# Kernel optimization log

Measured on AMD Instinct MI355X. Metric: run time of the kernel, lower is better.

Reference implementation:

```python
import jax, jax.numpy as jnp
import numpy as np

NUM_NODES = 20000
NUM_EDGES = 65536
WIDTH = 64
EDGE_FEAT = 6
HIDDEN = 128


def setup_inputs() -> dict:
    key = jax.random.key(0)
    ks = jax.random.split(key, 6)
    x = jax.random.normal(ks[0], (NUM_NODES, WIDTH), dtype=jnp.float32)
    edge_attr = jax.random.normal(ks[1], (NUM_EDGES, EDGE_FEAT), dtype=jnp.float32)
    # weight-generating MLP params (the `nn` callable), fan-in scaled
    W1 = jax.random.normal(ks[2], (EDGE_FEAT, HIDDEN), dtype=jnp.float32) / np.sqrt(EDGE_FEAT)
    b1 = jnp.zeros((HIDDEN,), dtype=jnp.float32)
    W2 = jax.random.normal(ks[3], (HIDDEN, WIDTH * WIDTH), dtype=jnp.float32) / np.sqrt(HIDDEN)
    b2 = jnp.zeros((WIDTH * WIDTH,), dtype=jnp.float32)
    senders = jax.random.randint(ks[4], (NUM_EDGES,), 0, NUM_NODES)
    receivers = jax.random.randint(ks[5], (NUM_EDGES,), 0, NUM_NODES)
    return {"x": x, "edge_attr": edge_attr, "W1": W1, "b1": b1,
            "W2": W2, "b2": b2, "senders": senders, "receivers": receivers}


def reference(x, edge_attr, W1, b1, W2, b2, senders, receivers):
    n_segs, width = x.shape
    # nn(edge_attr): (E, width*width) edge-conditioned weights
    h = jax.nn.relu(edge_attr @ W1 + b1)
    weight = (h @ W2 + b2).reshape(-1, width, width)  # (E, w, w)
    # gather sender features, per-edge (1,w) @ (w,w) matmul -> (E, w)
    msgs = jnp.einsum('ew,ewv->ev', x[senders], weight)
    # scatter-sum messages into receiver nodes (aggr == 'sum')
    return jax.ops.segment_sum(msgs, receivers, num_segments=n_segs)
```

## Files before the change

### kernel.cpp

```cpp
#include <hip/hip_runtime.h>
#include <stdint.h>

typedef _Float16 f16;
typedef f16 f16x8 __attribute__((ext_vector_type(8)));
typedef float f32x4 __attribute__((ext_vector_type(4)));

#define NUM_NODES 20000
#define NUM_EDGES 65536
#define WIDTH 64
#define EDGE_FEAT 6
#define HIDDEN 128
#define BM 256
#define NCHUNK 129
#define XPAD 72

#define XH_HALFS (NUM_NODES * WIDTH)
#define XCONV_BLKS 625

__global__ __launch_bounds__(256) void prep_kernel(
    const float* __restrict__ x, const float* __restrict__ W2,
    const float* __restrict__ b2, f16* __restrict__ ws_h)
{
  __shared__ float row[4096];
  f16* x_h = ws_h;
  f16* W2g = ws_h + XH_HALFS;
  const int blk = blockIdx.x, tid = threadIdx.x;

  if (blk < NCHUNK) {
    const int ki = blk;
    const float* srcrow;
    if (ki < HIDDEN) {
      const float4* src = (const float4*)(W2 + (size_t)ki * 4096);
      #pragma unroll
      for (int i = 0; i < 4; ++i) {
        float4 v = src[tid + 256 * i];
        *(float4*)&row[(tid + 256 * i) * 4] = v;
      }
      __syncthreads();
      srcrow = row;
    } else {
      srcrow = b2;
    }
    const int obase = tid * 16;
    f16x8 outv0, outv1;
    #pragma unroll
    for (int u = 0; u < 8; ++u) {
      int o = obase + u;
      int n = o >> 6, pg = (o >> 3) & 7, j = o & 7;
      int k = (pg ^ (n & 7)) * 8 + j;
      outv0[u] = (f16)srcrow[k * 64 + n];
    }
    #pragma unroll
    for (int u = 0; u < 8; ++u) {
      int o = obase + 8 + u;
      int n = o >> 6, pg = (o >> 3) & 7, j = o & 7;
      int k = (pg ^ (n & 7)) * 8 + j;
      outv1[u] = (f16)srcrow[k * 64 + n];
    }
    *(f16x8*)&W2g[(size_t)ki * 4096 + obase] = outv0;
    *(f16x8*)&W2g[(size_t)ki * 4096 + obase + 8] = outv1;
  } else {
    int idx = (blk - NCHUNK) * 2048 + tid * 8;
    if (idx + 8 <= XH_HALFS) {
      float4 a = *(const float4*)(x + idx);
      float4 b = *(const float4*)(x + idx + 4);
      f16x8 hv;
      hv[0] = (f16)a.x; hv[1] = (f16)a.y; hv[2] = (f16)a.z; hv[3] = (f16)a.w;
      hv[4] = (f16)b.x; hv[5] = (f16)b.y; hv[6] = (f16)b.z; hv[7] = (f16)b.w;
      *(f16x8*)&x_h[idx] = hv;
    }
  }
}

__global__ __launch_bounds__(256, 2) void nnconv_kernel(
    const float* __restrict__ ea, const float* __restrict__ W1,
    const float* __restrict__ b1, const int* __restrict__ senders,
    const int* __restrict__ receivers, const f16* __restrict__ ws_h,
    float* __restrict__ out)
{
  const f16* x_h = ws_h;
  const f16* W2g = ws_h + XH_HALFS;
  __shared__ __align__(16) f16 xt[BM][XPAD];
  __shared__ __align__(16) f16 Bb[2][4096];

  const int tid = threadIdx.x;
  const int lane = tid & 63, wid = tid >> 6;
  const int quad = lane >> 4, l15 = lane & 15;
  const int chunk = blockIdx.x & 255;
  const int khalf = blockIdx.x >> 8;
  const int k0 = khalf ? 65 : 0;
  const int kcount = khalf ? 64 : 65;
  const int e0 = chunk * BM;
  const int rowbase = wid * 64;

  {
    int s = senders[e0 + tid];
    const uint4* src = (const uint4*)(x_h + (size_t)s * WIDTH);
    uint4* dst = (uint4*)&xt[tid][0];
    #pragma unroll
    for (int i = 0; i < 8; ++i) dst[i] = src[i];
  }

  float ear[4][6];
  #pragma unroll
  for (int t = 0; t < 4; ++t) {
    const float* p = ea + (size_t)(e0 + rowbase + t * 16 + l15) * EDGE_FEAT;
    #pragma unroll
    for (int f = 0; f < 6; ++f) ear[t][f] = p[f];
  }

  int boff[2][4];
  #pragma unroll
  for (int kc = 0; kc < 2; ++kc)
    #pragma unroll
    for (int nt = 0; nt < 4; ++nt) {
      int n = nt * 16 + l15;
      int g = kc * 4 + quad;
      boff[kc][nt] = n * 64 + (g ^ (n & 7)) * 8;
    }

  uint4 pre0 = *(const uint4*)(W2g + (size_t)k0 * 4096 + tid * 8);
  uint4 pre1 = *(const uint4*)(W2g + (size_t)k0 * 4096 + 2048 + tid * 8);

  __syncthreads();

  f16x8 xf[4][2];
  #pragma unroll
  for (int t = 0; t < 4; ++t)
    #pragma unroll
    for (int kc = 0; kc < 2; ++kc)
      xf[t][kc] = *(const f16x8*)&xt[rowbase + t * 16 + l15][kc * 32 + quad * 8];

  f32x4 acc[4][4];
  #pragma unroll
  for (int t = 0; t < 4; ++t)
    #pragma unroll
    for (int nt = 0; nt < 4; ++nt)
      acc[t][nt] = (f32x4){0.f, 0.f, 0.f, 0.f};

  for (int kk = 0; kk < kcount; ++kk) {
    const int ki = k0 + kk;
    f16* buf = &Bb[kk & 1][0];
    *(uint4*)&buf[tid * 8] = pre0;
    *(uint4*)&buf[2048 + tid * 8] = pre1;
    if (kk + 1 < kcount) {
      pre0 = *(const uint4*)(W2g + (size_t)(ki + 1) * 4096 + tid * 8);
      pre1 = *(const uint4*)(W2g + (size_t)(ki + 1) * 4096 + 2048 + tid * 8);
    }

    f16 hv[4];
    if (ki < HIDDEN) {
      float b1c = b1[ki];
      float w1c[6];
      #pragma unroll
      for (int f = 0; f < 6; ++f) w1c[f] = W1[f * HIDDEN + ki];
      #pragma unroll
      for (int t = 0; t < 4; ++t) {
        float s = b1c;
        #pragma unroll
        for (int f = 0; f < 6; ++f) s = fmaf(ear[t][f], w1c[f], s);
        hv[t] = (f16)fmaxf(s, 0.f);
      }
    } else {
      #pragma unroll
      for (int t = 0; t < 4; ++t) hv[t] = (f16)1.f;
    }

    __syncthreads();

    f16x8 bf[2][4];
    #pragma unroll
    for (int kc = 0; kc < 2; ++kc)
      #pragma unroll
      for (int nt = 0; nt < 4; ++nt)
        bf[kc][nt] = *(const f16x8*)&buf[boff[kc][nt]];

    #pragma unroll
    for (int t = 0; t < 4; ++t) {
      f16x8 sa0 = xf[t][0] * hv[t];
      f16x8 sa1 = xf[t][1] * hv[t];
      #pragma unroll
      for (int nt = 0; nt < 4; ++nt) {
        acc[t][nt] = __builtin_amdgcn_mfma_f32_16x16x32_f16(sa0, bf[0][nt], acc[t][nt], 0, 0, 0);
        acc[t][nt] = __builtin_amdgcn_mfma_f32_16x16x32_f16(sa1, bf[1][nt], acc[t][nt], 0, 0, 0);
      }
    }
  }

  #pragma unroll
  for (int t = 0; t < 4; ++t) {
    int ebase = e0 + rowbase + t * 16 + quad * 4;
    int rc[4];
    #pragma unroll
    for (int r = 0; r < 4; ++r) rc[r] = receivers[ebase + r];
    #pragma unroll
    for (int nt = 0; nt < 4; ++nt) {
      int v = nt * 16 + l15;
      #pragma unroll
      for (int r = 0; r < 4; ++r)
        atomicAdd(out + (size_t)rc[r] * WIDTH + v, acc[t][nt][r]);
    }
  }
}

extern "C" void kernel_launch(void* const* d_in, const int* in_sizes, int n_in,
                              void* d_out, int out_size, void* d_ws, size_t ws_size,
                              hipStream_t stream) {
  const float* x  = (const float*)d_in[0];
  const float* ea = (const float*)d_in[1];
  const float* W1 = (const float*)d_in[2];
  const float* b1 = (const float*)d_in[3];
  const float* W2 = (const float*)d_in[4];
  const float* b2 = (const float*)d_in[5];
  const int* snd  = (const int*)d_in[6];
  const int* rcv  = (const int*)d_in[7];
  float* out = (float*)d_out;
  f16* wsh = (f16*)d_ws;

  hipMemsetAsync(d_out, 0, (size_t)out_size * sizeof(float), stream);
  prep_kernel<<<NCHUNK + XCONV_BLKS, 256, 0, stream>>>(x, W2, b2, wsh);
  nnconv_kernel<<<2 * (NUM_EDGES / BM), 256, 0, stream>>>(ea, W1, b1, snd, rcv, wsh, out);
}
```

Before: 150.8 us.

## Precompute hidden activations in prep pass and stream W2 fragments directly to registers

```diff
diff --git a/kernel.cpp b/kernel.cpp
--- a/kernel.cpp
+++ b/kernel.cpp
@@ -16,17 +16,23 @@
 
 #define XH_HALFS (NUM_NODES * WIDTH)
 #define XCONV_BLKS 625
+#define W2G_HALFS (NCHUNK * 4096)
+#define HT_HALFS ((size_t)NCHUNK * NUM_EDGES)
+#define HBLKS (NUM_EDGES / 256)
 
 __global__ __launch_bounds__(256) void prep_kernel(
     const float* __restrict__ x, const float* __restrict__ W2,
-    const float* __restrict__ b2, f16* __restrict__ ws_h)
+    const float* __restrict__ b2, const float* __restrict__ ea,
+    const float* __restrict__ W1, const float* __restrict__ b1,
+    f16* __restrict__ ws_h)
 {
-  __shared__ float row[4096];
   f16* x_h = ws_h;
   f16* W2g = ws_h + XH_HALFS;
+  f16* hT  = ws_h + XH_HALFS + W2G_HALFS;
   const int blk = blockIdx.x, tid = threadIdx.x;
 
   if (blk < NCHUNK) {
+    __shared__ float row[4096];
     const int ki = blk;
     const float* srcrow;
     if (ki < HIDDEN) {
@@ -59,7 +65,7 @@
     }
     *(f16x8*)&W2g[(size_t)ki * 4096 + obase] = outv0;
     *(f16x8*)&W2g[(size_t)ki * 4096 + obase + 8] = outv1;
-  } else {
+  } else if (blk < NCHUNK + XCONV_BLKS) {
     int idx = (blk - NCHUNK) * 2048 + tid * 8;
     if (idx + 8 <= XH_HALFS) {
       float4 a = *(const float4*)(x + idx);
@@ -69,9 +75,29 @@
       hv[4] = (f16)b.x; hv[5] = (f16)b.y; hv[6] = (f16)b.z; hv[7] = (f16)b.w;
       *(f16x8*)&x_h[idx] = hv;
     }
+  } else {
+    __shared__ float w1s[EDGE_FEAT * HIDDEN];
+    __shared__ float b1s[HIDDEN];
+    for (int i = tid; i < EDGE_FEAT * HIDDEN; i += 256) w1s[i] = W1[i];
+    if (tid < HIDDEN) b1s[tid] = b1[tid];
+    __syncthreads();
+    const int e = (blk - NCHUNK - XCONV_BLKS) * 256 + tid;
+    const float* p = ea + (size_t)e * EDGE_FEAT;
+    float a[6];
+    #pragma unroll
+    for (int f = 0; f < 6; ++f) a[f] = p[f];
+    #pragma unroll 4
+    for (int k = 0; k < HIDDEN; ++k) {
+      float s = b1s[k];
+      #pragma unroll
+      for (int f = 0; f < 6; ++f) s = fmaf(a[f], w1s[f * HIDDEN + k], s);
+      hT[(size_t)k * NUM_EDGES + e] = (f16)fmaxf(s, 0.f);
+    }
+    hT[(size_t)HIDDEN * NUM_EDGES + e] = (f16)1.f;
   }
 }
 
+template<int HT>
 __global__ __launch_bounds__(256, 2) void nnconv_kernel(
     const float* __restrict__ ea, const float* __restrict__ W1,
     const float* __restrict__ b1, const int* __restrict__ senders,
@@ -80,8 +106,8 @@
 {
   const f16* x_h = ws_h;
   const f16* W2g = ws_h + XH_HALFS;
+  const f16* hT  = ws_h + XH_HALFS + W2G_HALFS;
   __shared__ __align__(16) f16 xt[BM][XPAD];
-  __shared__ __align__(16) f16 Bb[2][4096];
 
   const int tid = threadIdx.x;
   const int lane = tid & 63, wid = tid >> 6;
@@ -102,11 +128,13 @@
   }
 
   float ear[4][6];
-  #pragma unroll
-  for (int t = 0; t < 4; ++t) {
-    const float* p = ea + (size_t)(e0 + rowbase + t * 16 + l15) * EDGE_FEAT;
-    #pragma unroll
-    for (int f = 0; f < 6; ++f) ear[t][f] = p[f];
+  if (!HT) {
+    #pragma unroll
+    for (int t = 0; t < 4; ++t) {
+      const float* p = ea + (size_t)(e0 + rowbase + t * 16 + l15) * EDGE_FEAT;
+      #pragma unroll
+      for (int f = 0; f < 6; ++f) ear[t][f] = p[f];
+    }
   }
 
   int boff[2][4];
@@ -119,8 +147,23 @@
       boff[kc][nt] = n * 64 + (g ^ (n & 7)) * 8;
     }
 
-  uint4 pre0 = *(const uint4*)(W2g + (size_t)k0 * 4096 + tid * 8);
-  uint4 pre1 = *(const uint4*)(W2g + (size_t)k0 * 4096 + 2048 + tid * 8);
+  const int hrow = e0 + rowbase + l15;
+
+  f16x8 bc[2][4];
+  f16 hc[4];
+  {
+    const f16* Bp = W2g + (size_t)k0 * 4096;
+    #pragma unroll
+    for (int kc = 0; kc < 2; ++kc)
+      #pragma unroll
+      for (int nt = 0; nt < 4; ++nt)
+        bc[kc][nt] = *(const f16x8*)(Bp + boff[kc][nt]);
+    if (HT) {
+      const f16* hp = hT + (size_t)k0 * NUM_EDGES + hrow;
+      #pragma unroll
+      for (int t = 0; t < 4; ++t) hc[t] = hp[t * 16];
+    }
+  }
 
   __syncthreads();
 
@@ -140,40 +183,46 @@
 
   for (int kk = 0; kk < kcount; ++kk) {
     const int ki = k0 + kk;
-    f16* buf = &Bb[kk & 1][0];
-    *(uint4*)&buf[tid * 8] = pre0;
-    *(uint4*)&buf[2048 + tid * 8] = pre1;
-    if (kk + 1 < kcount) {
-      pre0 = *(const uint4*)(W2g + (size_t)(ki + 1) * 4096 + tid * 8);
-      pre1 = *(const uint4*)(W2g + (size_t)(ki + 1) * 4096 + 2048 + tid * 8);
+    const int kin = (kk + 1 < kcount) ? ki + 1 : ki;
+
+    f16x8 bn[2][4];
+    f16 hn[4];
+    {
+      const f16* Bp = W2g + (size_t)kin * 4096;
+      #pragma unroll
+      for (int kc = 0; kc < 2; ++kc)
+        #pragma unroll
+        for (int nt = 0; nt < 4; ++nt)
+          bn[kc][nt] = *(const f16x8*)(Bp + boff[kc][nt]);
+      if (HT) {
+        const f16* hp = hT + (size_t)kin * NUM_EDGES + hrow;
+        #pragma unroll
+        for (int t = 0; t < 4; ++t) hn[t] = hp[t * 16];
+      }
     }
 
     f16 hv[4];
-    if (ki < HIDDEN) {
-      float b1c = b1[ki];
-      float w1c[6];
-      #pragma unroll
-      for (int f = 0; f < 6; ++f) w1c[f] = W1[f * HIDDEN + ki];
-      #pragma unroll
-      for (int t = 0; t < 4; ++t) {
-        float s = b1c;
-        #pragma unroll
-        for (int f = 0; f < 6; ++f) s = fmaf(ear[t][f], w1c[f], s);
-        hv[t] = (f16)fmaxf(s, 0.f);
-      }
+    if (HT) {
+      #pragma unroll
+      for (int t = 0; t < 4; ++t) hv[t] = hc[t];
     } else {
-      #pragma unroll
-      for (int t = 0; t < 4; ++t) hv[t] = (f16)1.f;
-    }
-
-    __syncthreads();
-
-    f16x8 bf[2][4];
-    #pragma unroll
-    for (int kc = 0; kc < 2; ++kc)
-      #pragma unroll
-      for (int nt = 0; nt < 4; ++nt)
-        bf[kc][nt] = *(const f16x8*)&buf[boff[kc][nt]];
+      if (ki < HIDDEN) {
+        float b1c = b1[ki];
+        float w1c[6];
+        #pragma unroll
+        for (int f = 0; f < 6; ++f) w1c[f] = W1[f * HIDDEN + ki];
+        #pragma unroll
+        for (int t = 0; t < 4; ++t) {
+          float s = b1c;
+          #pragma unroll
+          for (int f = 0; f < 6; ++f) s = fmaf(ear[t][f], w1c[f], s);
+          hv[t] = (f16)fmaxf(s, 0.f);
+        }
+      } else {
+        #pragma unroll
+        for (int t = 0; t < 4; ++t) hv[t] = (f16)1.f;
+      }
+    }
 
     #pragma unroll
     for (int t = 0; t < 4; ++t) {
@@ -181,9 +230,19 @@
       f16x8 sa1 = xf[t][1] * hv[t];
       #pragma unroll
       for (int nt = 0; nt < 4; ++nt) {
-        acc[t][nt] = __builtin_amdgcn_mfma_f32_16x16x32_f16(sa0, bf[0][nt], acc[t][nt], 0, 0, 0);
-        acc[t][nt] = __builtin_amdgcn_mfma_f32_16x16x32_f16(sa1, bf[1][nt], acc[t][nt], 0, 0, 0);
-      }
+        acc[t][nt] = __builtin_amdgcn_mfma_f32_16x16x32_f16(sa0, bc[0][nt], acc[t][nt], 0, 0, 0);
+        acc[t][nt] = __builtin_amdgcn_mfma_f32_16x16x32_f16(sa1, bc[1][nt], acc[t][nt], 0, 0, 0);
+      }
+    }
+
+    #pragma unroll
+    for (int kc = 0; kc < 2; ++kc)
+      #pragma unroll
+      for (int nt = 0; nt < 4; ++nt)
+        bc[kc][nt] = bn[kc][nt];
+    if (HT) {
+      #pragma unroll
+      for (int t = 0; t < 4; ++t) hc[t] = hn[t];
     }
   }
 
@@ -217,7 +276,14 @@
   float* out = (float*)d_out;
   f16* wsh = (f16*)d_ws;
 
+  const size_t need = ((size_t)XH_HALFS + W2G_HALFS + HT_HALFS) * sizeof(f16);
+  const int use_ht = (ws_size >= need) ? 1 : 0;
+
   hipMemsetAsync(d_out, 0, (size_t)out_size * sizeof(float), stream);
-  prep_kernel<<<NCHUNK + XCONV_BLKS, 256, 0, stream>>>(x, W2, b2, wsh);
-  nnconv_kernel<<<2 * (NUM_EDGES / BM), 256, 0, stream>>>(ea, W1, b1, snd, rcv, wsh, out);
+  const int prep_grid = NCHUNK + XCONV_BLKS + (use_ht ? HBLKS : 0);
+  prep_kernel<<<prep_grid, 256, 0, stream>>>(x, W2, b2, ea, W1, b1, wsh);
+  if (use_ht)
+    nnconv_kernel<1><<<2 * (NUM_EDGES / BM), 256, 0, stream>>>(ea, W1, b1, snd, rcv, wsh, out);
+  else
+    nnconv_kernel<0><<<2 * (NUM_EDGES / BM), 256, 0, stream>>>(ea, W1, b1, snd, rcv, wsh, out);
 }
```

Measured after the change: 176.5 us. 1.17x slower.

## Restructure NNConv main loop with 8-wave blocks and async LDS staging of W2

Applied to the files above, without the earlier changes.

```diff
diff --git a/kernel.cpp b/kernel.cpp
--- a/kernel.cpp
+++ b/kernel.cpp
@@ -11,23 +11,41 @@
 #define EDGE_FEAT 6
 #define HIDDEN 128
 #define BM 256
-#define NCHUNK 129
+#define PADCH 132
 #define XPAD 72
 
 #define XH_HALFS (NUM_NODES * WIDTH)
 #define XCONV_BLKS 625
+#define W2G_HALFS (PADCH * 4096)
+#define OUT_FLOATS (NUM_NODES * WIDTH)
+#define ZBLKS 313
+
+__device__ __forceinline__ void gload_lds16(const f16* g, f16* l) {
+  __builtin_amdgcn_global_load_lds(
+      (const __attribute__((address_space(1))) unsigned int*)g,
+      (__attribute__((address_space(3))) unsigned int*)l, 16, 0, 0);
+}
 
 __global__ __launch_bounds__(256) void prep_kernel(
     const float* __restrict__ x, const float* __restrict__ W2,
-    const float* __restrict__ b2, f16* __restrict__ ws_h)
+    const float* __restrict__ b2, f16* __restrict__ ws_h,
+    float* __restrict__ out)
 {
-  __shared__ float row[4096];
   f16* x_h = ws_h;
   f16* W2g = ws_h + XH_HALFS;
   const int blk = blockIdx.x, tid = threadIdx.x;
 
-  if (blk < NCHUNK) {
+  if (blk < PADCH) {
     const int ki = blk;
+    if (ki > HIDDEN) {
+      f16x8 z;
+      #pragma unroll
+      for (int u = 0; u < 8; ++u) z[u] = (f16)0.f;
+      *(f16x8*)&W2g[(size_t)ki * 4096 + tid * 16] = z;
+      *(f16x8*)&W2g[(size_t)ki * 4096 + tid * 16 + 8] = z;
+      return;
+    }
+    __shared__ float row[4096];
     const float* srcrow;
     if (ki < HIDDEN) {
       const float4* src = (const float4*)(W2 + (size_t)ki * 4096);
@@ -59,8 +77,8 @@
     }
     *(f16x8*)&W2g[(size_t)ki * 4096 + obase] = outv0;
     *(f16x8*)&W2g[(size_t)ki * 4096 + obase + 8] = outv1;
-  } else {
-    int idx = (blk - NCHUNK) * 2048 + tid * 8;
+  } else if (blk < PADCH + XCONV_BLKS) {
+    int idx = (blk - PADCH) * 2048 + tid * 8;
     if (idx + 8 <= XH_HALFS) {
       float4 a = *(const float4*)(x + idx);
       float4 b = *(const float4*)(x + idx + 4);
@@ -69,10 +87,18 @@
       hv[4] = (f16)b.x; hv[5] = (f16)b.y; hv[6] = (f16)b.z; hv[7] = (f16)b.w;
       *(f16x8*)&x_h[idx] = hv;
     }
-  }
-}
-
-__global__ __launch_bounds__(256, 2) void nnconv_kernel(
+  } else {
+    int base = (blk - PADCH - XCONV_BLKS) * 4096 + tid * 16;
+    float4 z = {0.f, 0.f, 0.f, 0.f};
+    #pragma unroll
+    for (int i = 0; i < 4; ++i) {
+      int idx = base + i * 4;
+      if (idx + 4 <= OUT_FLOATS) *(float4*)(out + idx) = z;
+    }
+  }
+}
+
+__global__ __launch_bounds__(512, 1) void nnconv_kernel(
     const float* __restrict__ ea, const float* __restrict__ W1,
     const float* __restrict__ b1, const int* __restrict__ senders,
     const int* __restrict__ receivers, const f16* __restrict__ ws_h,
@@ -81,47 +107,53 @@
   const f16* x_h = ws_h;
   const f16* W2g = ws_h + XH_HALFS;
   __shared__ __align__(16) f16 xt[BM][XPAD];
-  __shared__ __align__(16) f16 Bb[2][4096];
+  __shared__ __align__(16) f16 Bring[2 * 16384];
 
   const int tid = threadIdx.x;
   const int lane = tid & 63, wid = tid >> 6;
   const int quad = lane >> 4, l15 = lane & 15;
-  const int chunk = blockIdx.x & 255;
-  const int khalf = blockIdx.x >> 8;
-  const int k0 = khalf ? 65 : 0;
-  const int kcount = khalf ? 64 : 65;
-  const int e0 = chunk * BM;
-  const int rowbase = wid * 64;
+  const int mquad = wid >> 1, nhalf = wid & 1;
+  const int e0 = blockIdx.x * BM;
+  const int mbase = mquad * 64;
+  f16* BrF = &Bring[0];
+
+#define STAGE(GIDX, GP)                                                       \
+  {                                                                           \
+    _Pragma("unroll") for (int i_ = 0; i_ < 4; ++i_) {                        \
+      int slice_ = wid + 8 * i_;                                              \
+      gload_lds16(W2g + (size_t)(GIDX) * 16384 + slice_ * 512 + (lane << 3),  \
+                  BrF + (GP) * 16384 + slice_ * 512);                         \
+    }                                                                         \
+  }
+  STAGE(0, 0);
 
   {
-    int s = senders[e0 + tid];
-    const uint4* src = (const uint4*)(x_h + (size_t)s * WIDTH);
-    uint4* dst = (uint4*)&xt[tid][0];
-    #pragma unroll
-    for (int i = 0; i < 8; ++i) dst[i] = src[i];
+    int r = tid >> 1, half = tid & 1;
+    int s = senders[e0 + r];
+    const uint4* src = (const uint4*)(x_h + (size_t)s * WIDTH + half * 32);
+    uint4* dst = (uint4*)&xt[r][half * 32];
+    #pragma unroll
+    for (int i = 0; i < 4; ++i) dst[i] = src[i];
   }
 
   float ear[4][6];
   #pragma unroll
   for (int t = 0; t < 4; ++t) {
-    const float* p = ea + (size_t)(e0 + rowbase + t * 16 + l15) * EDGE_FEAT;
+    const float* p = ea + (size_t)(e0 + mbase + t * 16 + l15) * EDGE_FEAT;
     #pragma unroll
     for (int f = 0; f < 6; ++f) ear[t][f] = p[f];
   }
 
-  int boff[2][4];
+  int boff[2][2];
   #pragma unroll
   for (int kc = 0; kc < 2; ++kc)
     #pragma unroll
-    for (int nt = 0; nt < 4; ++nt) {
-      int n = nt * 16 + l15;
+    for (int nt = 0; nt < 2; ++nt) {
+      int n = (nhalf * 2 + nt) * 16 + l15;
       int g = kc * 4 + quad;
       boff[kc][nt] = n * 64 + (g ^ (n & 7)) * 8;
     }
 
-  uint4 pre0 = *(const uint4*)(W2g + (size_t)k0 * 4096 + tid * 8);
-  uint4 pre1 = *(const uint4*)(W2g + (size_t)k0 * 4096 + 2048 + tid * 8);
-
   __syncthreads();
 
   f16x8 xf[4][2];
@@ -129,73 +161,105 @@
   for (int t = 0; t < 4; ++t)
     #pragma unroll
     for (int kc = 0; kc < 2; ++kc)
-      xf[t][kc] = *(const f16x8*)&xt[rowbase + t * 16 + l15][kc * 32 + quad * 8];
-
-  f32x4 acc[4][4];
+      xf[t][kc] = *(const f16x8*)&xt[mbase + t * 16 + l15][kc * 32 + quad * 8];
+
+  f32x4 acc[4][2];
   #pragma unroll
   for (int t = 0; t < 4; ++t)
     #pragma unroll
-    for (int nt = 0; nt < 4; ++nt)
+    for (int nt = 0; nt < 2; ++nt)
       acc[t][nt] = (f32x4){0.f, 0.f, 0.f, 0.f};
 
-  for (int kk = 0; kk < kcount; ++kk) {
-    const int ki = k0 + kk;
-    f16* buf = &Bb[kk & 1][0];
-    *(uint4*)&buf[tid * 8] = pre0;
-    *(uint4*)&buf[2048 + tid * 8] = pre1;
-    if (kk + 1 < kcount) {
-      pre0 = *(const uint4*)(W2g + (size_t)(ki + 1) * 4096 + tid * 8);
-      pre1 = *(const uint4*)(W2g + (size_t)(ki + 1) * 4096 + 2048 + tid * 8);
-    }
-
-    f16 hv[4];
-    if (ki < HIDDEN) {
-      float b1c = b1[ki];
-      float w1c[6];
-      #pragma unroll
-      for (int f = 0; f < 6; ++f) w1c[f] = W1[f * HIDDEN + ki];
-      #pragma unroll
-      for (int t = 0; t < 4; ++t) {
-        float s = b1c;
-        #pragma unroll
-        for (int f = 0; f < 6; ++f) s = fmaf(ear[t][f], w1c[f], s);
-        hv[t] = (f16)fmaxf(s, 0.f);
+#define RD(DST, CBASE)                                                        \
+  _Pragma("unroll") for (int kc = 0; kc < 2; ++kc)                            \
+    _Pragma("unroll") for (int nt = 0; nt < 2; ++nt)                          \
+      DST[kc][nt] = *(const f16x8*)&(CBASE)[boff[kc][nt]];
+
+#define MM(BF, HV)                                                            \
+  __builtin_amdgcn_s_setprio(1);                                              \
+  _Pragma("unroll") for (int t = 0; t < 4; ++t) {                             \
+    f16x8 sa0_ = xf[t][0] * HV[t];                                            \
+    f16x8 sa1_ = xf[t][1] * HV[t];                                            \
+    _Pragma("unroll") for (int nt = 0; nt < 2; ++nt) {                        \
+      acc[t][nt] = __builtin_amdgcn_mfma_f32_16x16x32_f16(                    \
+          sa0_, BF[0][nt], acc[t][nt], 0, 0, 0);                              \
+      acc[t][nt] = __builtin_amdgcn_mfma_f32_16x16x32_f16(                    \
+          sa1_, BF[1][nt], acc[t][nt], 0, 0, 0);                              \
+    }                                                                         \
+  }                                                                           \
+  __builtin_amdgcn_s_setprio(0);
+
+#define HCOMP(KI, HV)                                                         \
+  {                                                                           \
+    float b1c_ = b1[(KI)];                                                    \
+    float w1c_[6];                                                            \
+    _Pragma("unroll") for (int f = 0; f < 6; ++f)                             \
+      w1c_[f] = W1[f * HIDDEN + (KI)];                                        \
+    _Pragma("unroll") for (int t = 0; t < 4; ++t) {                           \
+      float s_ = b1c_;                                                        \
+      _Pragma("unroll") for (int f = 0; f < 6; ++f)                           \
+        s_ = fmaf(ear[t][f], w1c_[f], s_);                                    \
+      HV[t] = (f16)fmaxf(s_, 0.f);                                            \
+    }                                                                         \
+  }
+
+  #pragma unroll 1
+  for (int g = 0; g < 32; ++g) {
+    asm volatile("s_waitcnt vmcnt(0) lgkmcnt(0)\n\ts_barrier" ::: "memory");
+    __builtin_amdgcn_sched_barrier(0);
+    STAGE(g + 1, (g + 1) & 1);
+    __builtin_amdgcn_sched_barrier(0);
+
+    f16* gb = BrF + (g & 1) * 16384;
+    const int kb = g * 4;
+    f16 h0[4], h1[4], h2[4], h3[4];
+    HCOMP(kb + 0, h0);
+    HCOMP(kb + 1, h1);
+    HCOMP(kb + 2, h2);
+    HCOMP(kb + 3, h3);
+
+    f16x8 bfP[2][2], bfQ[2][2];
+    RD(bfP, gb);
+    RD(bfQ, gb + 4096);
+    MM(bfP, h0);
+    RD(bfP, gb + 8192);
+    MM(bfQ, h1);
+    RD(bfQ, gb + 12288);
+    MM(bfP, h2);
+    MM(bfQ, h3);
+  }
+
+  asm volatile("s_waitcnt vmcnt(0) lgkmcnt(0)\n\ts_barrier" ::: "memory");
+  __builtin_amdgcn_sched_barrier(0);
+  {
+    f16x8 bfP[2][2];
+    RD(bfP, BrF);
+    __builtin_amdgcn_s_setprio(1);
+    #pragma unroll
+    for (int t = 0; t < 4; ++t)
+      #pragma unroll
+      for (int nt = 0; nt < 2; ++nt) {
+        acc[t][nt] = __builtin_amdgcn_mfma_f32_16x16x32_f16(
+            xf[t][0], bfP[0][nt], acc[t][nt], 0, 0, 0);
+        acc[t][nt] = __builtin_amdgcn_mfma_f32_16x16x32_f16(
+            xf[t][1], bfP[1][nt], acc[t][nt], 0, 0, 0);
       }
-    } else {
-      #pragma unroll
-      for (int t = 0; t < 4; ++t) hv[t] = (f16)1.f;
-    }
-
-    __syncthreads();
-
-    f16x8 bf[2][4];
-    #pragma unroll
-    for (int kc = 0; kc < 2; ++kc)
-      #pragma unroll
-      for (int nt = 0; nt < 4; ++nt)
-        bf[kc][nt] = *(const f16x8*)&buf[boff[kc][nt]];
-
-    #pragma unroll
-    for (int t = 0; t < 4; ++t) {
-      f16x8 sa0 = xf[t][0] * hv[t];
-      f16x8 sa1 = xf[t][1] * hv[t];
-      #pragma unroll
-      for (int nt = 0; nt < 4; ++nt) {
-        acc[t][nt] = __builtin_amdgcn_mfma_f32_16x16x32_f16(sa0, bf[0][nt], acc[t][nt], 0, 0, 0);
-        acc[t][nt] = __builtin_amdgcn_mfma_f32_16x16x32_f16(sa1, bf[1][nt], acc[t][nt], 0, 0, 0);
-      }
-    }
-  }
+    __builtin_amdgcn_s_setprio(0);
+  }
+#undef STAGE
+#undef RD
+#undef MM
+#undef HCOMP
 
   #pragma unroll
   for (int t = 0; t < 4; ++t) {
-    int ebase = e0 + rowbase + t * 16 + quad * 4;
+    int ebase = e0 + mbase + t * 16 + quad * 4;
     int rc[4];
     #pragma unroll
     for (int r = 0; r < 4; ++r) rc[r] = receivers[ebase + r];
     #pragma unroll
-    for (int nt = 0; nt < 4; ++nt) {
-      int v = nt * 16 + l15;
+    for (int nt = 0; nt < 2; ++nt) {
+      int v = (nhalf * 2 + nt) * 16 + l15;
       #pragma unroll
       for (int r = 0; r < 4; ++r)
         atomicAdd(out + (size_t)rc[r] * WIDTH + v, acc[t][nt][r]);
@@ -217,7 +281,7 @@
   float* out = (float*)d_out;
   f16* wsh = (f16*)d_ws;
 
-  hipMemsetAsync(d_out, 0, (size_t)out_size * sizeof(float), stream);
-  prep_kernel<<<NCHUNK + XCONV_BLKS, 256, 0, stream>>>(x, W2, b2, wsh);
-  nnconv_kernel<<<2 * (NUM_EDGES / BM), 256, 0, stream>>>(ea, W1, b1, snd, rcv, wsh, out);
-}
+  const int prep_grid = PADCH + XCONV_BLKS + ZBLKS;
+  prep_kernel<<<prep_grid, 256, 0, stream>>>(x, W2, b2, wsh, out);
+  nnconv_kernel<<<NUM_EDGES / BM, 512, 0, stream>>>(ea, W1, b1, snd, rcv, wsh, out);
+}
```

After: 147.0 us. -2.5%, faster.
